# Optimization experiments

Hardware: AMD Instinct MI355X
Metric: run time of the kernel (lower is better)

Reference implementation:

```python
import jax, jax.numpy as jnp
import numpy as np


def _add_self_loops(edge_index, num_nodes):
    loops = jnp.arange(num_nodes, dtype=edge_index.dtype)
    row = jnp.concatenate([edge_index[0], loops])
    col = jnp.concatenate([edge_index[1], loops])
    return row, col


def _gcn_norm(row, col, num_nodes):
    # deg computed at aggregation targets (col), edge weights all 1 (PyG gcn_norm)
    deg = jax.ops.segment_sum(jnp.ones_like(col, dtype=jnp.float32), col,
                              num_segments=num_nodes)
    dinv = jnp.where(deg > 0, jax.lax.rsqrt(deg), 0.0)
    return dinv[row] * dinv[col]  # [E+N]


def _gcn_conv(x, row, col, norm, W, b, num_nodes):
    h = x @ W                                  # [N, out] linear first (PyG GCNConv)
    msg = h[row] * norm[:, None]               # gather + scale, [E+N, out]
    agg = jax.ops.segment_sum(msg, col, num_segments=num_nodes)
    return agg + b


def setup_inputs() -> dict:
    key = jax.random.key(0)
    N, F, H, E = 100000, 128, 64, 1600000
    k1, k2, k3, k4 = jax.random.split(key, 4)
    x = jax.random.normal(k1, (N, F), dtype=jnp.float32)
    edge_index = jax.random.randint(k2, (2, E), 0, N, dtype=jnp.int64)
    s1 = 1.0 / np.sqrt(F)
    s2 = 1.0 / np.sqrt(H)
    W1 = jax.random.normal(k3, (F, H), dtype=jnp.float32) * s1
    b1 = jnp.zeros((H,), dtype=jnp.float32)
    W2 = jax.random.normal(k4, (H, 1), dtype=jnp.float32) * s2
    b2 = jnp.zeros((1,), dtype=jnp.float32)
    return {"x": x, "edge_index": edge_index, "W1": W1, "b1": b1,
            "W2": W2, "b2": b2}


def reference(x, edge_index, W1, b1, W2, b2):
    N = x.shape[0]
    row, col = _add_self_loops(edge_index, N)
    norm = _gcn_norm(row, col, N)
    h = jax.nn.relu(_gcn_conv(x, row, col, norm, W1, b1, N))
    # dropout p=0.0 -> identity
    out = _gcn_conv(h, row, col, norm, W2, b2, N)
    return out.reshape(-1)  # [N]
```

## Files before the change

kernel.cpp:

```cpp
#include <hip/hip_runtime.h>
#include <hip/hip_bf16.h>


#define SHIFT 8
#define BMASK ((1 << SHIFT) - 1)
#define MAXB 512

typedef __attribute__((ext_vector_type(8))) short bf16x8;
typedef __attribute__((ext_vector_type(4))) float f32x4;

__device__ __forceinline__ bool detect_i64(const unsigned* u) {
    unsigned acc = 0;
#pragma unroll
    for (int i = 1; i <= 32; ++i) acc |= u[2 * i + 1];
    return acc == 0u;
}

__device__ __forceinline__ int load_edge(const void* ei, bool is64, long long idx) {
    if (is64) return ((const int*)ei)[idx << 1];
    return ((const int*)ei)[idx];
}

__device__ __forceinline__ unsigned bf16_rn(float x) {
    unsigned u = __float_as_uint(x);
    return (u + 0x7fffu + ((u >> 16) & 1u)) >> 16;
}
__device__ __forceinline__ unsigned pack_bf2(float a, float b) {
    return bf16_rn(a) | (bf16_rn(b) << 16);
}
__device__ __forceinline__ float bflo(unsigned v) { return __uint_as_float(v << 16); }
__device__ __forceinline__ float bfhi(unsigned v) {
    return __uint_as_float(v & 0xffff0000u);
}

__global__ __launch_bounds__(256) void binA_kernel(const void* ei, int* gcursor,
                                                   unsigned* __restrict__ pairs, int E,
                                                   int cap, int NB) {
    bool is64 = detect_i64((const unsigned*)ei);
    __shared__ int whist[4][MAXB];
    __shared__ int bcur[MAXB];
    int t = threadIdx.x;
    int wid = t >> 6;
    long long per = ((long long)E + gridDim.x - 1) / gridDim.x;
    long long e0 = (long long)blockIdx.x * per;
    long long e1 = e0 + per;
    if (e1 > E) e1 = E;
    for (int b = t; b < NB; b += 256) {
        whist[0][b] = 0; whist[1][b] = 0; whist[2][b] = 0; whist[3][b] = 0;
    }
    __syncthreads();
    unsigned pk[16];
    int bs[16];
    int i = 0;
    for (long long e = e0 + t; e < e1; e += 256, ++i) {
        int r = load_edge(ei, is64, e);
        int c = load_edge(ei, is64, (long long)E + e);
        int b = c >> SHIFT;
        unsigned p = ((unsigned)r << SHIFT) | (unsigned)(c & BMASK);
        atomicAdd(&whist[wid][b], 1);
        if (i < 16) { pk[i] = p; bs[i] = b; }
    }
    __syncthreads();
    for (int b = t; b < NB; b += 256) {
        int tot = whist[0][b] + whist[1][b] + whist[2][b] + whist[3][b];
        int rel = tot ? atomicAdd(&gcursor[b], tot) : 0;
        bcur[b] = b * cap + rel;
    }
    __syncthreads();
    i = 0;
    for (long long e = e0 + t; e < e1; e += 256, ++i) {
        unsigned p;
        int b;
        if (i < 16) {
            p = pk[i];
            b = bs[i];
        } else {
            int r = load_edge(ei, is64, e);
            int c = load_edge(ei, is64, (long long)E + e);
            b = c >> SHIFT;
            p = ((unsigned)r << SHIFT) | (unsigned)(c & BMASK);
        }
        int rk = atomicAdd(&bcur[b], 1);
        pairs[rk] = p;
    }
}

__global__ __launch_bounds__(256) void binB_kernel(const unsigned* __restrict__ pairs,
                                                   const int* __restrict__ gcursor,
                                                   int* __restrict__ csr,
                                                   int* __restrict__ offs,
                                                   int* __restrict__ deg, int N,
                                                   int cap) {
    __shared__ int cnt[256];
    __shared__ int cur[256];
    __shared__ int tmp[256];
    int b = blockIdx.x, t = threadIdx.x;
    int start = b * cap, end = start + gcursor[b];
    cnt[t] = 0;
    __syncthreads();
    for (int i = start + t; i < end; i += 256) atomicAdd(&cnt[pairs[i] & BMASK], 1);
    __syncthreads();
    int c0 = cnt[t];
    tmp[t] = c0;
    __syncthreads();
    for (int off = 1; off < 256; off <<= 1) {
        int xv = (t >= off) ? tmp[t - off] : 0;
        __syncthreads();
        tmp[t] += xv;
        __syncthreads();
    }
    int p0 = start + tmp[t] - c0;
    cur[t] = p0;
    int node = (b << SHIFT) + t;
    if (node < N) {
        offs[node] = p0;
        deg[node] = c0;
    }
    __syncthreads();
    for (int i = start + t; i < end; i += 256) {
        unsigned p = pairs[i];
        int pos = atomicAdd(&cur[p & BMASK], 1);
        csr[pos] = (int)(p >> SHIFT);
    }
}

__global__ __launch_bounds__(256) void gemm1_kernel(const float* __restrict__ x,
                                                    const float* __restrict__ W1,
                                                    const int* __restrict__ deg,
                                                    unsigned* __restrict__ hs_u, int N) {
    __shared__ alignas(16) char smem[32768];
    char* wt_hi = smem;
    char* wt_lo = smem + 16384;
    int t = threadIdx.x;
    int l = t & 63;
    int w = t >> 6;

#pragma unroll
    for (int i = 0; i < 32; ++i) {
        int idx = t + 256 * i;
        int k = idx >> 6;
        int c = idx & 63;
        float f = W1[idx];
        unsigned uh = bf16_rn(f);
        float fh = __uint_as_float(uh << 16);
        unsigned ul = bf16_rn(f - fh);
        int byte = c * 256 + (((k >> 3) ^ (c & 15)) << 4) + ((k & 7) << 1);
        *(unsigned short*)(wt_hi + byte) = (unsigned short)uh;
        *(unsigned short*)(wt_lo + byte) = (unsigned short)ul;
    }
    __syncthreads();

    int row0 = blockIdx.x * 64 + w * 16;
    int arow = row0 + (l & 15);
    bool rok = arow < N;
    const f32x4* x4 = (const f32x4*)x;

    f32x4 acc[4];
#pragma unroll
    for (int ct = 0; ct < 4; ++ct) acc[ct] = (f32x4)(0.f);

#pragma unroll
    for (int ks = 0; ks < 4; ++ks) {
        int kbase = ks * 32 + (l >> 4) * 8;
        f32x4 xa = (f32x4)(0.f), xb = (f32x4)(0.f);
        if (rok) {
            xa = x4[(size_t)arow * 32 + (kbase >> 2)];
            xb = x4[(size_t)arow * 32 + (kbase >> 2) + 1];
        }
        unsigned ah[4], al[4];
#pragma unroll
        for (int j = 0; j < 4; ++j) {
            float f0 = (j < 2) ? ((j == 0) ? xa.x : xa.z) : ((j == 2) ? xb.x : xb.z);
            float f1 = (j < 2) ? ((j == 0) ? xa.y : xa.w) : ((j == 2) ? xb.y : xb.w);
            unsigned h0 = bf16_rn(f0), h1 = bf16_rn(f1);
            float r0 = f0 - __uint_as_float(h0 << 16);
            float r1 = f1 - __uint_as_float(h1 << 16);
            ah[j] = h0 | (h1 << 16);
            al[j] = bf16_rn(r0) | (bf16_rn(r1) << 16);
        }
        bf16x8 Ah, Al;
        ((unsigned*)&Ah)[0] = ah[0]; ((unsigned*)&Ah)[1] = ah[1];
        ((unsigned*)&Ah)[2] = ah[2]; ((unsigned*)&Ah)[3] = ah[3];
        ((unsigned*)&Al)[0] = al[0]; ((unsigned*)&Al)[1] = al[1];
        ((unsigned*)&Al)[2] = al[2]; ((unsigned*)&Al)[3] = al[3];
        int chunk = ks * 4 + (l >> 4);
#pragma unroll
        for (int ct = 0; ct < 4; ++ct) {
            int col = ct * 16 + (l & 15);
            int byte = col * 256 + ((chunk ^ (col & 15)) << 4);
            bf16x8 Bh = *(const bf16x8*)(wt_hi + byte);
            bf16x8 Bl = *(const bf16x8*)(wt_lo + byte);
            acc[ct] = __builtin_amdgcn_mfma_f32_16x16x32_bf16(Ah, Bh, acc[ct], 0, 0, 0);
            acc[ct] = __builtin_amdgcn_mfma_f32_16x16x32_bf16(Ah, Bl, acc[ct], 0, 0, 0);
            acc[ct] = __builtin_amdgcn_mfma_f32_16x16x32_bf16(Al, Bh, acc[ct], 0, 0, 0);
        }
    }

    __syncthreads();
    float* hsb = (float*)(smem) + w * 16 * 68;
#pragma unroll
    for (int ct = 0; ct < 4; ++ct) {
#pragma unroll
        for (int i = 0; i < 4; ++i) {
            int row = (l >> 4) * 4 + i;
            hsb[row * 68 + ct * 16 + (l & 15)] = acc[ct][i];
        }
    }
    __syncthreads();
    int row = l & 15;
    int q = l >> 4;
    int gr = row0 + row;
    if (gr < N) {
        float dinv = rsqrtf((float)deg[gr] + 1.0f);
        const f32x4* src = (const f32x4*)(hsb + row * 68 + q * 16);
        f32x4 f0 = src[0], f1 = src[1], f2 = src[2], f3 = src[3];
        uint4 o0, o1;
        o0.x = pack_bf2(f0.x * dinv, f0.y * dinv);
        o0.y = pack_bf2(f0.z * dinv, f0.w * dinv);
        o0.z = pack_bf2(f1.x * dinv, f1.y * dinv);
        o0.w = pack_bf2(f1.z * dinv, f1.w * dinv);
        o1.x = pack_bf2(f2.x * dinv, f2.y * dinv);
        o1.y = pack_bf2(f2.z * dinv, f2.w * dinv);
        o1.z = pack_bf2(f3.x * dinv, f3.y * dinv);
        o1.w = pack_bf2(f3.z * dinv, f3.w * dinv);
        uint4* dst = (uint4*)&hs_u[(size_t)gr * 32 + q * 8];
        dst[0] = o0;
        dst[1] = o1;
    }
}

#define ACCV(v)                                            \
    {                                                      \
        float2 t0 = make_float2(bflo((v).x), bfhi((v).x)); \
        float2 t1 = make_float2(bflo((v).y), bfhi((v).y)); \
        float2 t2 = make_float2(bflo((v).z), bfhi((v).z)); \
        float2 t3 = make_float2(bflo((v).w), bfhi((v).w)); \
        a0.x += t0.x; a0.y += t0.y;                        \
        a1.x += t1.x; a1.y += t1.y;                        \
        a2.x += t2.x; a2.y += t2.y;                        \
        a3.x += t3.x; a3.y += t3.y;                        \
    }

__global__ __launch_bounds__(256) void pull1_kernel(
    const uint4* __restrict__ hs4, const int* __restrict__ offs,
    const int* __restrict__ deg, const int* __restrict__ csr,
    const float* __restrict__ b1, const float* __restrict__ W2,
    float* __restrict__ hs2, int N) {
    int gid = blockIdx.x * blockDim.x + threadIdx.x;
    int w = gid >> 3;
    if (w >= N) return;
    int lane = threadIdx.x & 63;
    int k = lane & 7;
    int s = offs[w];
    int cnt = deg[w];
    float dinv = rsqrtf((float)cnt + 1.0f);
    float2 a0 = make_float2(0.f, 0.f), a1 = a0, a2 = a0, a3 = a0;
    {
        uint4 v = hs4[(size_t)w * 8 + k];
        ACCV(v);
    }
    int e = 0;
    for (; e + 8 <= cnt; e += 8) {
        int r0 = csr[s + e + 0];
        int r1 = csr[s + e + 1];
        int r2 = csr[s + e + 2];
        int r3 = csr[s + e + 3];
        int r4 = csr[s + e + 4];
        int r5 = csr[s + e + 5];
        int r6 = csr[s + e + 6];
        int r7 = csr[s + e + 7];
        uint4 v0 = hs4[(size_t)r0 * 8 + k];
        uint4 v1 = hs4[(size_t)r1 * 8 + k];
        uint4 v2 = hs4[(size_t)r2 * 8 + k];
        uint4 v3 = hs4[(size_t)r3 * 8 + k];
        uint4 v4 = hs4[(size_t)r4 * 8 + k];
        uint4 v5 = hs4[(size_t)r5 * 8 + k];
        uint4 v6 = hs4[(size_t)r6 * 8 + k];
        uint4 v7 = hs4[(size_t)r7 * 8 + k];
        ACCV(v0); ACCV(v1); ACCV(v2); ACCV(v3);
        ACCV(v4); ACCV(v5); ACCV(v6); ACCV(v7);
    }
    for (; e < cnt; ++e) {
        int r = csr[s + e];
        uint4 v = hs4[(size_t)r * 8 + k];
        ACCV(v);
    }
    float4 bA = ((const float4*)b1)[2 * k];
    float4 bB = ((const float4*)b1)[2 * k + 1];
    float4 wA = ((const float4*)W2)[2 * k];
    float4 wB = ((const float4*)W2)[2 * k + 1];
    float p = fmaxf(fmaf(dinv, a0.x, bA.x), 0.f) * wA.x
            + fmaxf(fmaf(dinv, a0.y, bA.y), 0.f) * wA.y
            + fmaxf(fmaf(dinv, a1.x, bA.z), 0.f) * wA.z
            + fmaxf(fmaf(dinv, a1.y, bA.w), 0.f) * wA.w
            + fmaxf(fmaf(dinv, a2.x, bB.x), 0.f) * wB.x
            + fmaxf(fmaf(dinv, a2.y, bB.y), 0.f) * wB.y
            + fmaxf(fmaf(dinv, a3.x, bB.z), 0.f) * wB.z
            + fmaxf(fmaf(dinv, a3.y, bB.w), 0.f) * wB.w;
    p += __shfl_xor(p, 1);
    p += __shfl_xor(p, 2);
    p += __shfl_xor(p, 4);
    if ((lane & 7) == 0) hs2[w] = dinv * p;
}

__global__ __launch_bounds__(256) void pull2_kernel(
    const float* __restrict__ hs2, const int* __restrict__ offs,
    const int* __restrict__ deg, const int* __restrict__ csr,
    const float* __restrict__ b2, float* __restrict__ out, int N) {
    int i = blockIdx.x * blockDim.x + threadIdx.x;
    if (i >= N) return;
    int s = offs[i];
    int cnt = deg[i];
    float dinv = rsqrtf((float)cnt + 1.0f);
    float a0 = hs2[i];
    float a1 = 0.f, a2 = 0.f, a3 = 0.f;
    float a4 = 0.f, a5 = 0.f, a6 = 0.f, a7 = 0.f;
    int kk = 0;
    for (; kk + 8 <= cnt; kk += 8) {
        a0 += hs2[csr[s + kk]];
        a1 += hs2[csr[s + kk + 1]];
        a2 += hs2[csr[s + kk + 2]];
        a3 += hs2[csr[s + kk + 3]];
        a4 += hs2[csr[s + kk + 4]];
        a5 += hs2[csr[s + kk + 5]];
        a6 += hs2[csr[s + kk + 6]];
        a7 += hs2[csr[s + kk + 7]];
    }
    for (; kk < cnt; ++kk) a0 += hs2[csr[s + kk]];
    out[i] = fmaf(dinv, ((a0 + a1) + (a2 + a3)) + ((a4 + a5) + (a6 + a7)), b2[0]);
}

extern "C" void kernel_launch(void* const* d_in, const int* in_sizes, int n_in,
                              void* d_out, int out_size, void* d_ws, size_t ws_size,
                              hipStream_t stream) {
    const float* x = (const float*)d_in[0];
    const void* ei = d_in[1];
    const float* W1 = (const float*)d_in[2];
    const float* b1 = (const float*)d_in[3];
    const float* W2 = (const float*)d_in[4];
    const float* b2 = (const float*)d_in[5];
    float* out = (float*)d_out;

    int N = in_sizes[0] / 128;
    int E = in_sizes[1] / 2;
    int NB = (N + (1 << SHIFT) - 1) >> SHIFT;
    int cap = ((2 * (E / NB)) / 256 + 2) * 256;

    char* p = (char*)d_ws;
    unsigned* hs_u = (unsigned*)p;  p += (size_t)N * 32 * sizeof(unsigned);
    float* hs2 = (float*)p;         p += (size_t)N * sizeof(float);
    int* offs = (int*)p;            p += (size_t)N * sizeof(int);
    int* deg = (int*)p;             p += (size_t)N * sizeof(int);
    unsigned* pairs = (unsigned*)p; p += (size_t)NB * cap * sizeof(unsigned);
    int* csr = (int*)p;             p += (size_t)NB * cap * sizeof(int);
    int* gcursor = (int*)p;         p += MAXB * sizeof(int);

    (void)hipMemsetAsync(gcursor, 0, MAXB * sizeof(int), stream);
    binA_kernel<<<512, 256, 0, stream>>>(ei, gcursor, pairs, E, cap, NB);
    binB_kernel<<<NB, 256, 0, stream>>>(pairs, gcursor, csr, offs, deg, N, cap);
    gemm1_kernel<<<(N + 63) / 64, 256, 0, stream>>>(x, W1, deg, hs_u, N);
    pull1_kernel<<<((size_t)N * 8 + 255) / 256, 256, 0, stream>>>(
        (const uint4*)hs_u, offs, deg, csr, b1, W2, hs2, N);
    pull2_kernel<<<(N + 255) / 256, 256, 0, stream>>>(hs2, offs, deg, csr, b2, out, N);
}
```

Baseline: 192.8 us.

## Fuse edge binning with GEMM1 and move dinv scaling into binB

Merges the edge-binning kernel and the first GEMM into one launch, with block indices selecting the role, so the two independent phases run concurrently and one launch is saved. The GEMM no longer needs degrees, so the dinv row scaling moves into binB, which reads and rewrites the bf16 hidden rows. This adds an extra read and write of the 12.8MB hidden buffer and a second bf16 rounding step. Separately, pull1 now loads CSR neighbor indices cooperatively once per 8 lanes, prefetches the next batch, and broadcasts them with shuffles instead of every lane reading all indices.

```diff
diff --git a/kernel.cpp b/kernel.cpp
--- a/kernel.cpp
+++ b/kernel.cpp
@@ -33,55 +33,155 @@
     return __uint_as_float(v & 0xffff0000u);
 }
 
-__global__ __launch_bounds__(256) void binA_kernel(const void* ei, int* gcursor,
-                                                   unsigned* __restrict__ pairs, int E,
-                                                   int cap, int NB) {
-    bool is64 = detect_i64((const unsigned*)ei);
-    __shared__ int whist[4][MAXB];
-    __shared__ int bcur[MAXB];
+__global__ __launch_bounds__(256) void fusedA_kernel(
+    const void* ei, int* gcursor, unsigned* __restrict__ pairs, int E, int cap, int NB,
+    const float* __restrict__ x, const float* __restrict__ W1,
+    unsigned* __restrict__ hs_u, int N, int nAblk) {
+    __shared__ alignas(16) char smem[32768];
     int t = threadIdx.x;
-    int wid = t >> 6;
-    long long per = ((long long)E + gridDim.x - 1) / gridDim.x;
-    long long e0 = (long long)blockIdx.x * per;
-    long long e1 = e0 + per;
-    if (e1 > E) e1 = E;
-    for (int b = t; b < NB; b += 256) {
-        whist[0][b] = 0; whist[1][b] = 0; whist[2][b] = 0; whist[3][b] = 0;
-    }
-    __syncthreads();
-    unsigned pk[16];
-    int bs[16];
-    int i = 0;
-    for (long long e = e0 + t; e < e1; e += 256, ++i) {
-        int r = load_edge(ei, is64, e);
-        int c = load_edge(ei, is64, (long long)E + e);
-        int b = c >> SHIFT;
-        unsigned p = ((unsigned)r << SHIFT) | (unsigned)(c & BMASK);
-        atomicAdd(&whist[wid][b], 1);
-        if (i < 16) { pk[i] = p; bs[i] = b; }
-    }
-    __syncthreads();
-    for (int b = t; b < NB; b += 256) {
-        int tot = whist[0][b] + whist[1][b] + whist[2][b] + whist[3][b];
-        int rel = tot ? atomicAdd(&gcursor[b], tot) : 0;
-        bcur[b] = b * cap + rel;
-    }
-    __syncthreads();
-    i = 0;
-    for (long long e = e0 + t; e < e1; e += 256, ++i) {
-        unsigned p;
-        int b;
-        if (i < 16) {
-            p = pk[i];
-            b = bs[i];
-        } else {
+    if ((int)blockIdx.x < nAblk) {
+        int* whist = (int*)smem;
+        int* bcur = (int*)(smem + 8192);
+        bool is64 = detect_i64((const unsigned*)ei);
+        int wid = t >> 6;
+        long long per = ((long long)E + nAblk - 1) / nAblk;
+        long long e0 = (long long)blockIdx.x * per;
+        long long e1 = e0 + per;
+        if (e1 > E) e1 = E;
+        for (int i = t; i < 4 * MAXB; i += 256) whist[i] = 0;
+        __syncthreads();
+        unsigned pk[16];
+        int bs[16];
+        int i = 0;
+        for (long long e = e0 + t; e < e1; e += 256, ++i) {
             int r = load_edge(ei, is64, e);
             int c = load_edge(ei, is64, (long long)E + e);
-            b = c >> SHIFT;
-            p = ((unsigned)r << SHIFT) | (unsigned)(c & BMASK);
-        }
-        int rk = atomicAdd(&bcur[b], 1);
-        pairs[rk] = p;
+            int b = c >> SHIFT;
+            unsigned p = ((unsigned)r << SHIFT) | (unsigned)(c & BMASK);
+            atomicAdd(&whist[wid * MAXB + b], 1);
+            if (i < 16) { pk[i] = p; bs[i] = b; }
+        }
+        __syncthreads();
+        for (int b = t; b < NB; b += 256) {
+            int tot = whist[b] + whist[MAXB + b] + whist[2 * MAXB + b] +
+                      whist[3 * MAXB + b];
+            int rel = tot ? atomicAdd(&gcursor[b], tot) : 0;
+            bcur[b] = b * cap + rel;
+        }
+        __syncthreads();
+        i = 0;
+        for (long long e = e0 + t; e < e1; e += 256, ++i) {
+            unsigned p;
+            int b;
+            if (i < 16) {
+                p = pk[i];
+                b = bs[i];
+            } else {
+                int r = load_edge(ei, is64, e);
+                int c = load_edge(ei, is64, (long long)E + e);
+                b = c >> SHIFT;
+                p = ((unsigned)r << SHIFT) | (unsigned)(c & BMASK);
+            }
+            int rk = atomicAdd(&bcur[b], 1);
+            pairs[rk] = p;
+        }
+    } else {
+        char* wt_hi = smem;
+        char* wt_lo = smem + 16384;
+        int l = t & 63;
+        int w = t >> 6;
+#pragma unroll
+        for (int i = 0; i < 32; ++i) {
+            int idx = t + 256 * i;
+            int k = idx >> 6;
+            int c = idx & 63;
+            float f = W1[idx];
+            unsigned uh = bf16_rn(f);
+            float fh = __uint_as_float(uh << 16);
+            unsigned ul = bf16_rn(f - fh);
+            int byte = c * 256 + (((k >> 3) ^ (c & 15)) << 4) + ((k & 7) << 1);
+            *(unsigned short*)(wt_hi + byte) = (unsigned short)uh;
+            *(unsigned short*)(wt_lo + byte) = (unsigned short)ul;
+        }
+        __syncthreads();
+        int row0 = ((int)blockIdx.x - nAblk) * 64 + w * 16;
+        int arow = row0 + (l & 15);
+        bool rok = arow < N;
+        const f32x4* x4 = (const f32x4*)x;
+        f32x4 acc[4];
+#pragma unroll
+        for (int ct = 0; ct < 4; ++ct) acc[ct] = (f32x4)(0.f);
+#pragma unroll
+        for (int ks = 0; ks < 4; ++ks) {
+            int kbase = ks * 32 + (l >> 4) * 8;
+            f32x4 xa = (f32x4)(0.f), xb = (f32x4)(0.f);
+            if (rok) {
+                xa = x4[(size_t)arow * 32 + (kbase >> 2)];
+                xb = x4[(size_t)arow * 32 + (kbase >> 2) + 1];
+            }
+            unsigned ah[4], al[4];
+#pragma unroll
+            for (int j = 0; j < 4; ++j) {
+                float f0 = (j < 2) ? ((j == 0) ? xa.x : xa.z)
+                                   : ((j == 2) ? xb.x : xb.z);
+                float f1 = (j < 2) ? ((j == 0) ? xa.y : xa.w)
+                                   : ((j == 2) ? xb.y : xb.w);
+                unsigned h0 = bf16_rn(f0), h1 = bf16_rn(f1);
+                float r0 = f0 - __uint_as_float(h0 << 16);
+                float r1 = f1 - __uint_as_float(h1 << 16);
+                ah[j] = h0 | (h1 << 16);
+                al[j] = bf16_rn(r0) | (bf16_rn(r1) << 16);
+            }
+            bf16x8 Ah, Al;
+            ((unsigned*)&Ah)[0] = ah[0]; ((unsigned*)&Ah)[1] = ah[1];
+            ((unsigned*)&Ah)[2] = ah[2]; ((unsigned*)&Ah)[3] = ah[3];
+            ((unsigned*)&Al)[0] = al[0]; ((unsigned*)&Al)[1] = al[1];
+            ((unsigned*)&Al)[2] = al[2]; ((unsigned*)&Al)[3] = al[3];
+            int chunk = ks * 4 + (l >> 4);
+#pragma unroll
+            for (int ct = 0; ct < 4; ++ct) {
+                int col = ct * 16 + (l & 15);
+                int byte = col * 256 + ((chunk ^ (col & 15)) << 4);
+                bf16x8 Bh = *(const bf16x8*)(wt_hi + byte);
+                bf16x8 Bl = *(const bf16x8*)(wt_lo + byte);
+                acc[ct] =
+                    __builtin_amdgcn_mfma_f32_16x16x32_bf16(Ah, Bh, acc[ct], 0, 0, 0);
+                acc[ct] =
+                    __builtin_amdgcn_mfma_f32_16x16x32_bf16(Ah, Bl, acc[ct], 0, 0, 0);
+                acc[ct] =
+                    __builtin_amdgcn_mfma_f32_16x16x32_bf16(Al, Bh, acc[ct], 0, 0, 0);
+            }
+        }
+        __syncthreads();
+        float* hsb = (float*)(smem) + w * 16 * 68;
+#pragma unroll
+        for (int ct = 0; ct < 4; ++ct) {
+#pragma unroll
+            for (int i = 0; i < 4; ++i) {
+                int row = (l >> 4) * 4 + i;
+                hsb[row * 68 + ct * 16 + (l & 15)] = acc[ct][i];
+            }
+        }
+        __syncthreads();
+        int row = l & 15;
+        int q = l >> 4;
+        int gr = row0 + row;
+        if (gr < N) {
+            const f32x4* src = (const f32x4*)(hsb + row * 68 + q * 16);
+            f32x4 f0 = src[0], f1 = src[1], f2 = src[2], f3 = src[3];
+            uint4 o0, o1;
+            o0.x = pack_bf2(f0.x, f0.y);
+            o0.y = pack_bf2(f0.z, f0.w);
+            o0.z = pack_bf2(f1.x, f1.y);
+            o0.w = pack_bf2(f1.z, f1.w);
+            o1.x = pack_bf2(f2.x, f2.y);
+            o1.y = pack_bf2(f2.z, f2.w);
+            o1.z = pack_bf2(f3.x, f3.y);
+            o1.w = pack_bf2(f3.z, f3.w);
+            uint4* dst = (uint4*)&hs_u[(size_t)gr * 32 + q * 8];
+            dst[0] = o0;
+            dst[1] = o1;
+        }
     }
 }
 
@@ -89,7 +189,8 @@
                                                    const int* __restrict__ gcursor,
                                                    int* __restrict__ csr,
                                                    int* __restrict__ offs,
-                                                   int* __restrict__ deg, int N,
+                                                   int* __restrict__ deg,
+                                                   unsigned* __restrict__ hs_u, int N,
                                                    int cap) {
     __shared__ int cnt[256];
     __shared__ int cur[256];
@@ -101,6 +202,14 @@
     for (int i = start + t; i < end; i += 256) atomicAdd(&cnt[pairs[i] & BMASK], 1);
     __syncthreads();
     int c0 = cnt[t];
+    int node = (b << SHIFT) + t;
+    bool nok = node < N;
+    uint4 hv[8];
+    if (nok) {
+        const uint4* src = (const uint4*)&hs_u[(size_t)node * 32];
+#pragma unroll
+        for (int i = 0; i < 8; ++i) hv[i] = src[i];
+    }
     tmp[t] = c0;
     __syncthreads();
     for (int off = 1; off < 256; off <<= 1) {
@@ -111,121 +220,26 @@
     }
     int p0 = start + tmp[t] - c0;
     cur[t] = p0;
-    int node = (b << SHIFT) + t;
-    if (node < N) {
+    if (nok) {
         offs[node] = p0;
         deg[node] = c0;
+        float dv = rsqrtf((float)c0 + 1.0f);
+        uint4* dst = (uint4*)&hs_u[(size_t)node * 32];
+#pragma unroll
+        for (int i = 0; i < 8; ++i) {
+            uint4 v = hv[i];
+            v.x = pack_bf2(bflo(v.x) * dv, bfhi(v.x) * dv);
+            v.y = pack_bf2(bflo(v.y) * dv, bfhi(v.y) * dv);
+            v.z = pack_bf2(bflo(v.z) * dv, bfhi(v.z) * dv);
+            v.w = pack_bf2(bflo(v.w) * dv, bfhi(v.w) * dv);
+            dst[i] = v;
+        }
     }
     __syncthreads();
     for (int i = start + t; i < end; i += 256) {
         unsigned p = pairs[i];
         int pos = atomicAdd(&cur[p & BMASK], 1);
         csr[pos] = (int)(p >> SHIFT);
-    }
-}
-
-__global__ __launch_bounds__(256) void gemm1_kernel(const float* __restrict__ x,
-                                                    const float* __restrict__ W1,
-                                                    const int* __restrict__ deg,
-                                                    unsigned* __restrict__ hs_u, int N) {
-    __shared__ alignas(16) char smem[32768];
-    char* wt_hi = smem;
-    char* wt_lo = smem + 16384;
-    int t = threadIdx.x;
-    int l = t & 63;
-    int w = t >> 6;
-
-#pragma unroll
-    for (int i = 0; i < 32; ++i) {
-        int idx = t + 256 * i;
-        int k = idx >> 6;
-        int c = idx & 63;
-        float f = W1[idx];
-        unsigned uh = bf16_rn(f);
-        float fh = __uint_as_float(uh << 16);
-        unsigned ul = bf16_rn(f - fh);
-        int byte = c * 256 + (((k >> 3) ^ (c & 15)) << 4) + ((k & 7) << 1);
-        *(unsigned short*)(wt_hi + byte) = (unsigned short)uh;
-        *(unsigned short*)(wt_lo + byte) = (unsigned short)ul;
-    }
-    __syncthreads();
-
-    int row0 = blockIdx.x * 64 + w * 16;
-    int arow = row0 + (l & 15);
-    bool rok = arow < N;
-    const f32x4* x4 = (const f32x4*)x;
-
-    f32x4 acc[4];
-#pragma unroll
-    for (int ct = 0; ct < 4; ++ct) acc[ct] = (f32x4)(0.f);
-
-#pragma unroll
-    for (int ks = 0; ks < 4; ++ks) {
-        int kbase = ks * 32 + (l >> 4) * 8;
-        f32x4 xa = (f32x4)(0.f), xb = (f32x4)(0.f);
-        if (rok) {
-            xa = x4[(size_t)arow * 32 + (kbase >> 2)];
-            xb = x4[(size_t)arow * 32 + (kbase >> 2) + 1];
-        }
-        unsigned ah[4], al[4];
-#pragma unroll
-        for (int j = 0; j < 4; ++j) {
-            float f0 = (j < 2) ? ((j == 0) ? xa.x : xa.z) : ((j == 2) ? xb.x : xb.z);
-            float f1 = (j < 2) ? ((j == 0) ? xa.y : xa.w) : ((j == 2) ? xb.y : xb.w);
-            unsigned h0 = bf16_rn(f0), h1 = bf16_rn(f1);
-            float r0 = f0 - __uint_as_float(h0 << 16);
-            float r1 = f1 - __uint_as_float(h1 << 16);
-            ah[j] = h0 | (h1 << 16);
-            al[j] = bf16_rn(r0) | (bf16_rn(r1) << 16);
-        }
-        bf16x8 Ah, Al;
-        ((unsigned*)&Ah)[0] = ah[0]; ((unsigned*)&Ah)[1] = ah[1];
-        ((unsigned*)&Ah)[2] = ah[2]; ((unsigned*)&Ah)[3] = ah[3];
-        ((unsigned*)&Al)[0] = al[0]; ((unsigned*)&Al)[1] = al[1];
-        ((unsigned*)&Al)[2] = al[2]; ((unsigned*)&Al)[3] = al[3];
-        int chunk = ks * 4 + (l >> 4);
-#pragma unroll
-        for (int ct = 0; ct < 4; ++ct) {
-            int col = ct * 16 + (l & 15);
-            int byte = col * 256 + ((chunk ^ (col & 15)) << 4);
-            bf16x8 Bh = *(const bf16x8*)(wt_hi + byte);
-            bf16x8 Bl = *(const bf16x8*)(wt_lo + byte);
-            acc[ct] = __builtin_amdgcn_mfma_f32_16x16x32_bf16(Ah, Bh, acc[ct], 0, 0, 0);
-            acc[ct] = __builtin_amdgcn_mfma_f32_16x16x32_bf16(Ah, Bl, acc[ct], 0, 0, 0);
-            acc[ct] = __builtin_amdgcn_mfma_f32_16x16x32_bf16(Al, Bh, acc[ct], 0, 0, 0);
-        }
-    }
-
-    __syncthreads();
-    float* hsb = (float*)(smem) + w * 16 * 68;
-#pragma unroll
-    for (int ct = 0; ct < 4; ++ct) {
-#pragma unroll
-        for (int i = 0; i < 4; ++i) {
-            int row = (l >> 4) * 4 + i;
-            hsb[row * 68 + ct * 16 + (l & 15)] = acc[ct][i];
-        }
-    }
-    __syncthreads();
-    int row = l & 15;
-    int q = l >> 4;
-    int gr = row0 + row;
-    if (gr < N) {
-        float dinv = rsqrtf((float)deg[gr] + 1.0f);
-        const f32x4* src = (const f32x4*)(hsb + row * 68 + q * 16);
-        f32x4 f0 = src[0], f1 = src[1], f2 = src[2], f3 = src[3];
-        uint4 o0, o1;
-        o0.x = pack_bf2(f0.x * dinv, f0.y * dinv);
-        o0.y = pack_bf2(f0.z * dinv, f0.w * dinv);
-        o0.z = pack_bf2(f1.x * dinv, f1.y * dinv);
-        o0.w = pack_bf2(f1.z * dinv, f1.w * dinv);
-        o1.x = pack_bf2(f2.x * dinv, f2.y * dinv);
-        o1.y = pack_bf2(f2.z * dinv, f2.w * dinv);
-        o1.z = pack_bf2(f3.x * dinv, f3.y * dinv);
-        o1.w = pack_bf2(f3.z * dinv, f3.w * dinv);
-        uint4* dst = (uint4*)&hs_u[(size_t)gr * 32 + q * 8];
-        dst[0] = o0;
-        dst[1] = o1;
     }
 }
 
@@ -251,6 +265,7 @@
     if (w >= N) return;
     int lane = threadIdx.x & 63;
     int k = lane & 7;
+    int lane8 = lane & 56;
     int s = offs[w];
     int cnt = deg[w];
     float dinv = rsqrtf((float)cnt + 1.0f);
@@ -259,29 +274,23 @@
         uint4 v = hs4[(size_t)w * 8 + k];
         ACCV(v);
     }
+    int rv = (k < cnt) ? csr[s + k] : 0;
     int e = 0;
-    for (; e + 8 <= cnt; e += 8) {
-        int r0 = csr[s + e + 0];
-        int r1 = csr[s + e + 1];
-        int r2 = csr[s + e + 2];
-        int r3 = csr[s + e + 3];
-        int r4 = csr[s + e + 4];
-        int r5 = csr[s + e + 5];
-        int r6 = csr[s + e + 6];
-        int r7 = csr[s + e + 7];
-        uint4 v0 = hs4[(size_t)r0 * 8 + k];
-        uint4 v1 = hs4[(size_t)r1 * 8 + k];
-        uint4 v2 = hs4[(size_t)r2 * 8 + k];
-        uint4 v3 = hs4[(size_t)r3 * 8 + k];
-        uint4 v4 = hs4[(size_t)r4 * 8 + k];
-        uint4 v5 = hs4[(size_t)r5 * 8 + k];
-        uint4 v6 = hs4[(size_t)r6 * 8 + k];
-        uint4 v7 = hs4[(size_t)r7 * 8 + k];
-        ACCV(v0); ACCV(v1); ACCV(v2); ACCV(v3);
-        ACCV(v4); ACCV(v5); ACCV(v6); ACCV(v7);
-    }
-    for (; e < cnt; ++e) {
-        int r = csr[s + e];
+    while (e + 8 <= cnt) {
+        int nx = e + 8 + k;
+        int rvn = (nx < cnt) ? csr[s + nx] : 0;
+#pragma unroll
+        for (int j = 0; j < 8; ++j) {
+            int r = __shfl(rv, lane8 + j);
+            uint4 v = hs4[(size_t)r * 8 + k];
+            ACCV(v);
+        }
+        rv = rvn;
+        e += 8;
+    }
+    int m = cnt - e;
+    for (int j = 0; j < m; ++j) {
+        int r = __shfl(rv, lane8 + j);
         uint4 v = hs4[(size_t)r * 8 + k];
         ACCV(v);
     }
@@ -345,6 +354,8 @@
     int E = in_sizes[1] / 2;
     int NB = (N + (1 << SHIFT) - 1) >> SHIFT;
     int cap = ((2 * (E / NB)) / 256 + 2) * 256;
+    int nAblk = 512;
+    int nGblk = (N + 63) / 64;
 
     char* p = (char*)d_ws;
     unsigned* hs_u = (unsigned*)p;  p += (size_t)N * 32 * sizeof(unsigned);
@@ -356,9 +367,9 @@
     int* gcursor = (int*)p;         p += MAXB * sizeof(int);
 
     (void)hipMemsetAsync(gcursor, 0, MAXB * sizeof(int), stream);
-    binA_kernel<<<512, 256, 0, stream>>>(ei, gcursor, pairs, E, cap, NB);
-    binB_kernel<<<NB, 256, 0, stream>>>(pairs, gcursor, csr, offs, deg, N, cap);
-    gemm1_kernel<<<(N + 63) / 64, 256, 0, stream>>>(x, W1, deg, hs_u, N);
+    fusedA_kernel<<<nAblk + nGblk, 256, 0, stream>>>(ei, gcursor, pairs, E, cap, NB, x,
+                                                     W1, hs_u, N, nAblk);
+    binB_kernel<<<NB, 256, 0, stream>>>(pairs, gcursor, csr, offs, deg, hs_u, N, cap);
     pull1_kernel<<<((size_t)N * 8 + 255) / 256, 256, 0, stream>>>(
         (const uint4*)hs_u, offs, deg, csr, b1, W2, hs2, N);
     pull2_kernel<<<(N + 255) / 256, 256, 0, stream>>>(hs2, offs, deg, csr, b2, out, N);
```

After: 188.0 us. 2.5% less time.
